# Kernel tuning notes

Measured on AMD Instinct MI355X. Metric: run time of the kernel, lower is better.

Reference implementation:

```python
import jax, jax.numpy as jnp
import numpy as np

N_NODES = 50000
N_EDGES = 1600000
D_FEAT = 128
EPS = 1e-12  # matches F.normalize clamp_min eps


def setup_inputs() -> dict:
    key = jax.random.key(0)
    k1, k2 = jax.random.split(key)
    x = jax.random.normal(k1, (N_NODES, D_FEAT), dtype=jnp.float32)
    beta = jnp.ones((1,), dtype=jnp.float32)  # AGNNConv learnable scalar, init 1.0
    edge_index = jax.random.randint(k2, (2, N_EDGES), 0, N_NODES, dtype=jnp.int64)
    return {"x": x, "beta": beta, "edge_index": edge_index}


def reference(x, beta, edge_index):
    N = x.shape[0]
    # AGNNConv default add_self_loops=True
    loop = jnp.arange(N, dtype=edge_index.dtype)
    src = jnp.concatenate([edge_index[0], loop])  # j (source / message sender)
    dst = jnp.concatenate([edge_index[1], loop])  # i (target / aggregator)

    # cosine-similarity attention logits per edge, scaled by beta
    xn = x * jax.lax.rsqrt(jnp.maximum(jnp.sum(x * x, axis=-1, keepdims=True), EPS * EPS))
    logits = beta[0] * jnp.sum(xn[src] * xn[dst], axis=-1)  # [E+N]

    # segment softmax over incoming edges of each target node
    m = jax.ops.segment_max(logits, dst, num_segments=N)
    m = jax.lax.stop_gradient(m)
    e = jnp.exp(logits - m[dst])
    s = jax.ops.segment_sum(e, dst, num_segments=N)
    alpha = e / s[dst]  # self-loops guarantee s > 0

    # scatter-aggregate messages alpha_e * x_src
    out = jax.ops.segment_sum(alpha[:, None] * x[src], dst, num_segments=N)

    # wrapper: activation (relu); normalization=False; dropout p=0 -> identity
    return jax.nn.relu(out)
```

## Files before the change

kernel.cpp:

```cpp
#include <hip/hip_runtime.h>

#define NN 50000
#define NE 1600000
#define DF 128
#define NB 1250
#define BSZ 40
#define CAP 1664
#define NWGP 512
#define CHKP 3125
#define NBF 3125

static __device__ __forceinline__ float bflo(unsigned int u) {
    unsigned int v = u << 16; float f; __builtin_memcpy(&f, &v, 4); return f;
}
static __device__ __forceinline__ float bfhi(unsigned int u) {
    unsigned int v = u & 0xFFFF0000u; float f; __builtin_memcpy(&f, &v, 4); return f;
}
static __device__ __forceinline__ unsigned int f2bf(float f) {
    unsigned int u; __builtin_memcpy(&u, &f, 4);
    u += 0x7FFFu + ((u >> 16) & 1u);
    return u >> 16;
}

static __device__ __forceinline__ int block_excl_scan512(int v, int t, int* wsum8) {
    int lane = t & 63, wv = t >> 6;
    int s = v;
    #pragma unroll
    for (int off = 1; off < 64; off <<= 1) {
        int u = __shfl_up(s, off);
        if (lane >= off) s += u;
    }
    if (lane == 63) wsum8[wv] = s;
    __syncthreads();
    int add = 0;
    #pragma unroll
    for (int w = 0; w < 8; ++w) add += (w < wv) ? wsum8[w] : 0;
    __syncthreads();
    return s + add - v;
}

static __device__ __forceinline__ int block_excl_scan256(int v, int t, int* wsum4) {
    int lane = t & 63, wv = t >> 6;
    int s = v;
    #pragma unroll
    for (int off = 1; off < 64; off <<= 1) {
        int u = __shfl_up(s, off);
        if (lane >= off) s += u;
    }
    if (lane == 63) wsum4[wv] = s;
    __syncthreads();
    int add = 0;
    #pragma unroll
    for (int w = 0; w < 4; ++w) add += (w < wv) ? wsum4[w] : 0;
    __syncthreads();
    return s + add - v;
}

__global__ __launch_bounds__(512)
void k_norm_part(const float* __restrict__ x,
                 const int* __restrict__ ei,
                 unsigned int* __restrict__ xn_bf,
                 float* __restrict__ norm,
                 unsigned int* __restrict__ descG,
                 unsigned int* __restrict__ pairs) {
    __shared__ int wsum8[8];
    __shared__ int cntL[NB];
    __shared__ int offL[NB];
    __shared__ unsigned int stg[CHKP];
    int t = threadIdx.x;
    if (blockIdx.x >= NWGP) {
        int nbid = blockIdx.x - NWGP;
        int l32 = t & 31;
        int node = nbid * 16 + ((t >> 6) << 1) + ((t & 63) >> 5);
        float4 v = ((const float4*)(x + (size_t)node * DF))[l32];
        float ss = v.x * v.x + v.y * v.y + v.z * v.z + v.w * v.w;
        #pragma unroll
        for (int m = 1; m < 32; m <<= 1) ss += __shfl_xor(ss, m);
        float rinv = rsqrtf(fmaxf(ss, 1e-24f));
        uint2 p;
        p.x = (f2bf(v.y * rinv) << 16) | f2bf(v.x * rinv);
        p.y = (f2bf(v.w * rinv) << 16) | f2bf(v.z * rinv);
        ((uint2*)(xn_bf + (size_t)node * 64))[l32] = p;
        if (l32 == 0) norm[node] = ss * rinv;
        return;
    }
    int wg = blockIdx.x;
    const int* srcp = ei + wg * CHKP;
    const int* dstp = ei + NE + wg * CHKP;
    for (int i = t; i < NB; i += 512) cntL[i] = 0;
    __syncthreads();
    #pragma unroll 4
    for (int i = t; i < CHKP; i += 512) atomicAdd(&cntL[dstp[i] / BSZ], 1);
    __syncthreads();
    {
        int base = t * 3;
        int loc[3];
        int s = 0;
        #pragma unroll
        for (int q = 0; q < 3; ++q) {
            int idx = base + q;
            int v = (idx < NB) ? cntL[idx] : 0;
            loc[q] = s;
            s += v;
        }
        int ex = block_excl_scan512(s, t, wsum8);
        #pragma unroll
        for (int q = 0; q < 3; ++q) {
            int idx = base + q;
            if (idx < NB) offL[idx] = ex + loc[q];
        }
    }
    __syncthreads();
    for (int i = t; i < NB; i += 512)
        descG[(size_t)wg * NB + i] = ((unsigned int)offL[i] << 16) | (unsigned int)cntL[i];
    __syncthreads();
    #pragma unroll 2
    for (int i = t; i < CHKP; i += 512) {
        int src = srcp[i];
        int dst = dstp[i];
        int b = dst / BSZ;
        int pos = atomicAdd(&offL[b], 1);
        stg[pos] = ((unsigned int)(dst - b * BSZ) << 16) | (unsigned int)src;
    }
    __syncthreads();
    unsigned int* chunk = pairs + (size_t)wg * CHKP;
    #pragma unroll 4
    for (int i = t; i < CHKP; i += 512) chunk[i] = stg[i];
}

__global__ __launch_bounds__(256)
void k_build_gather(const unsigned int* __restrict__ xn_bf,
                    const float* __restrict__ norm,
                    const unsigned int* __restrict__ descG,
                    const unsigned int* __restrict__ pairs,
                    const float* __restrict__ beta_p,
                    float* __restrict__ out) {
    __shared__ int wsum4[4];
    __shared__ int lenS[NWGP], offS[NWGP], rbase[NWGP];
    __shared__ unsigned int rawL[CAP];
    __shared__ unsigned int colL[CAP];
    __shared__ int hist[BSZ];
    __shared__ int rp[BSZ + 1];
    __shared__ int tot0, stotal;
    int b = blockIdx.x, t = threadIdx.x;

    unsigned int d0 = descG[(size_t)t * NB + b];
    unsigned int d1 = descG[(size_t)(t + 256) * NB + b];
    int len0 = (int)(d0 & 0xFFFFu), off0 = (int)(d0 >> 16);
    int len1 = (int)(d1 & 0xFFFFu), off1 = (int)(d1 >> 16);
    int rb0 = block_excl_scan256(len0, t, wsum4);
    if (t == 255) tot0 = rb0 + len0;
    int ex1 = block_excl_scan256(len1, t, wsum4);
    int rb1 = tot0 + ex1;
    if (t == 255) stotal = rb1 + len1;
    lenS[t] = len0;        offS[t] = off0;        rbase[t] = rb0;
    lenS[t + 256] = len1;  offS[t + 256] = off1;  rbase[t + 256] = rb1;
    if (t < BSZ) hist[t] = 0;
    __syncthreads();
    int cnt = stotal;
    if (cnt > CAP) cnt = CAP;

    int g16 = t >> 4, l16 = t & 15;
    for (int r = g16; r < NWGP; r += 16) {
        int len = lenS[r];
        int rb = rbase[r];
        const unsigned int* sp = pairs + (size_t)r * CHKP + offS[r];
        for (int q = l16; q < len; q += 16) {
            int pos = rb + q;
            if (pos < CAP) rawL[pos] = sp[q];
        }
    }
    __syncthreads();
    for (int i = t; i < cnt; i += 256) atomicAdd(&hist[rawL[i] >> 16], 1);
    __syncthreads();
    if (t < 64) {
        int v = (t < BSZ) ? hist[t] : 0;
        int s = v;
        #pragma unroll
        for (int off = 1; off < 64; off <<= 1) {
            int u = __shfl_up(s, off);
            if (t >= off) s += u;
        }
        if (t < BSZ) { rp[t + 1] = s; hist[t] = s - v; }
        if (t == 0) rp[0] = 0;
    }
    __syncthreads();
    for (int i = t; i < cnt; i += 256) {
        unsigned int p = rawL[i];
        unsigned int src = p & 0xFFFFu;
        int pos = atomicAdd(&hist[p >> 16], 1);
        colL[pos] = (f2bf(norm[src]) << 16) | src;
    }
    __syncthreads();

    int lane = t & 63;
    int w = t >> 6;
    int j = lane & 15;
    int g = lane >> 4;
    float beta = beta_p[0];
    float c = -fabsf(beta);
    for (int ln = w; ln < BSZ; ln += 4) {
        int node = b * BSZ + ln;
        uint4 du = ((const uint4*)(xn_bf + (size_t)node * 64))[j];
        float xd[8];
        #pragma unroll
        for (int q = 0; q < 4; ++q) {
            unsigned int u = (&du.x)[q];
            xd[2 * q]     = bflo(u);
            xd[2 * q + 1] = bfhi(u);
        }
        float acc[8] = {0.f, 0.f, 0.f, 0.f, 0.f, 0.f, 0.f, 0.f};
        float ssum = 0.f;
        int b0 = rp[ln], b1 = rp[ln + 1];

        int k = b0 + g;
        int kA = (k     < b1) ? k     : 0;
        int kB = (k + 4 < b1) ? k + 4 : 0;
        unsigned int pA = colL[kA];
        unsigned int pB = colL[kB];
        uint4 rA = ((const uint4*)(xn_bf + (size_t)(pA & 0xFFFFu) * 64))[j];
        uint4 rB = ((const uint4*)(xn_bf + (size_t)(pB & 0xFFFFu) * 64))[j];

        for (; k < b1; k += 8) {
            int kC = (k +  8 < b1) ? k +  8 : 0;
            int kD = (k + 12 < b1) ? k + 12 : 0;
            unsigned int pC = colL[kC];
            unsigned int pD = colL[kD];
            uint4 rC = ((const uint4*)(xn_bf + (size_t)(pC & 0xFFFFu) * 64))[j];
            uint4 rD = ((const uint4*)(xn_bf + (size_t)(pD & 0xFFFFu) * 64))[j];
            {
                float xs[8];
                #pragma unroll
                for (int q = 0; q < 4; ++q) {
                    unsigned int u = (&rA.x)[q];
                    xs[2 * q]     = bflo(u);
                    xs[2 * q + 1] = bfhi(u);
                }
                float dot = 0.f;
                #pragma unroll
                for (int q = 0; q < 8; ++q) dot = fmaf(xd[q], xs[q], dot);
                dot += __shfl_xor(dot, 1);
                dot += __shfl_xor(dot, 2);
                dot += __shfl_xor(dot, 4);
                dot += __shfl_xor(dot, 8);
                float e = __expf(fmaf(beta, dot, c));
                ssum += e;
                float wgt = e * bfhi(pA);
                #pragma unroll
                for (int q = 0; q < 8; ++q) acc[q] = fmaf(wgt, xs[q], acc[q]);
            }
            {
                float xs[8];
                #pragma unroll
                for (int q = 0; q < 4; ++q) {
                    unsigned int u = (&rB.x)[q];
                    xs[2 * q]     = bflo(u);
                    xs[2 * q + 1] = bfhi(u);
                }
                float dot = 0.f;
                #pragma unroll
                for (int q = 0; q < 8; ++q) dot = fmaf(xd[q], xs[q], dot);
                dot += __shfl_xor(dot, 1);
                dot += __shfl_xor(dot, 2);
                dot += __shfl_xor(dot, 4);
                dot += __shfl_xor(dot, 8);
                float e = __expf(fmaf(beta, dot, c));
                e = (k + 4 < b1) ? e : 0.f;
                ssum += e;
                float wgt = e * bfhi(pB);
                #pragma unroll
                for (int q = 0; q < 8; ++q) acc[q] = fmaf(wgt, xs[q], acc[q]);
            }
            pA = pC; pB = pD; rA = rC; rB = rD;
        }

        ssum += __shfl_xor(ssum, 16);
        ssum += __shfl_xor(ssum, 32);
        #pragma unroll
        for (int q = 0; q < 8; ++q) {
            acc[q] += __shfl_xor(acc[q], 16);
            acc[q] += __shfl_xor(acc[q], 32);
        }
        float e_self = __expf(beta + c);
        ssum += e_self;
        float wsl = e_self * norm[node];
        #pragma unroll
        for (int q = 0; q < 8; ++q) acc[q] = fmaf(wsl, xd[q], acc[q]);

        if (g == 0) {
            float inv = 1.0f / ssum;
            float4 o0, o1;
            o0.x = fmaxf(0.f, acc[0] * inv); o0.y = fmaxf(0.f, acc[1] * inv);
            o0.z = fmaxf(0.f, acc[2] * inv); o0.w = fmaxf(0.f, acc[3] * inv);
            o1.x = fmaxf(0.f, acc[4] * inv); o1.y = fmaxf(0.f, acc[5] * inv);
            o1.z = fmaxf(0.f, acc[6] * inv); o1.w = fmaxf(0.f, acc[7] * inv);
            float4* op = (float4*)(out + (size_t)node * DF + 8 * j);
            op[0] = o0;
            op[1] = o1;
        }
    }
}

extern "C" void kernel_launch(void* const* d_in, const int* in_sizes, int n_in,
                              void* d_out, int out_size, void* d_ws, size_t ws_size,
                              hipStream_t stream) {
    const float* x    = (const float*)d_in[0];
    const float* beta = (const float*)d_in[1];
    const int*   ei   = (const int*)d_in[2];
    float*       out  = (float*)d_out;

    char* ws = (char*)d_ws;
    unsigned int* xn_bf = (unsigned int*)ws;
    float* norm = (float*)(ws + 12800000);
    unsigned int* descG = (unsigned int*)(ws + 13000000);
    unsigned int* pairs = (unsigned int*)(ws + 15560000);

    k_norm_part  <<<NWGP + NBF, 512, 0, stream>>>(x, ei, xn_bf, norm, descG, pairs);
    k_build_gather<<<NB,        256, 0, stream>>>(xn_bf, norm, descG, pairs, beta, out);
}
```

Measured before the change: 162.1 us.

## Coarsen edge partition to 64 chunks and split normalization into own kernel

```diff
diff --git a/kernel.cpp b/kernel.cpp
--- a/kernel.cpp
+++ b/kernel.cpp
@@ -6,8 +6,8 @@
 #define NB 1250
 #define BSZ 40
 #define CAP 1664
-#define NWGP 512
-#define CHKP 3125
+#define NWGP 64
+#define CHKP 25000
 #define NBF 3125
 
 static __device__ __forceinline__ float bflo(unsigned int u) {
@@ -39,52 +39,15 @@
     return s + add - v;
 }
 
-static __device__ __forceinline__ int block_excl_scan256(int v, int t, int* wsum4) {
-    int lane = t & 63, wv = t >> 6;
-    int s = v;
-    #pragma unroll
-    for (int off = 1; off < 64; off <<= 1) {
-        int u = __shfl_up(s, off);
-        if (lane >= off) s += u;
-    }
-    if (lane == 63) wsum4[wv] = s;
-    __syncthreads();
-    int add = 0;
-    #pragma unroll
-    for (int w = 0; w < 4; ++w) add += (w < wv) ? wsum4[w] : 0;
-    __syncthreads();
-    return s + add - v;
-}
-
 __global__ __launch_bounds__(512)
-void k_norm_part(const float* __restrict__ x,
-                 const int* __restrict__ ei,
-                 unsigned int* __restrict__ xn_bf,
-                 float* __restrict__ norm,
-                 unsigned int* __restrict__ descG,
-                 unsigned int* __restrict__ pairs) {
+void k_part(const int* __restrict__ ei,
+            unsigned int* __restrict__ descG,
+            unsigned int* __restrict__ pairs) {
     __shared__ int wsum8[8];
     __shared__ int cntL[NB];
     __shared__ int offL[NB];
     __shared__ unsigned int stg[CHKP];
-    int t = threadIdx.x;
-    if (blockIdx.x >= NWGP) {
-        int nbid = blockIdx.x - NWGP;
-        int l32 = t & 31;
-        int node = nbid * 16 + ((t >> 6) << 1) + ((t & 63) >> 5);
-        float4 v = ((const float4*)(x + (size_t)node * DF))[l32];
-        float ss = v.x * v.x + v.y * v.y + v.z * v.z + v.w * v.w;
-        #pragma unroll
-        for (int m = 1; m < 32; m <<= 1) ss += __shfl_xor(ss, m);
-        float rinv = rsqrtf(fmaxf(ss, 1e-24f));
-        uint2 p;
-        p.x = (f2bf(v.y * rinv) << 16) | f2bf(v.x * rinv);
-        p.y = (f2bf(v.w * rinv) << 16) | f2bf(v.z * rinv);
-        ((uint2*)(xn_bf + (size_t)node * 64))[l32] = p;
-        if (l32 == 0) norm[node] = ss * rinv;
-        return;
-    }
-    int wg = blockIdx.x;
+    int wg = blockIdx.x, t = threadIdx.x;
     const int* srcp = ei + wg * CHKP;
     const int* dstp = ei + NE + wg * CHKP;
     for (int i = t; i < NB; i += 512) cntL[i] = 0;
@@ -128,6 +91,25 @@
     for (int i = t; i < CHKP; i += 512) chunk[i] = stg[i];
 }
 
+__global__ __launch_bounds__(512)
+void k_norm(const float* __restrict__ x,
+            unsigned int* __restrict__ xn_bf,
+            float* __restrict__ norm) {
+    int t = threadIdx.x;
+    int l32 = t & 31;
+    int node = blockIdx.x * 16 + (t >> 5);
+    float4 v = ((const float4*)(x + (size_t)node * DF))[l32];
+    float ss = v.x * v.x + v.y * v.y + v.z * v.z + v.w * v.w;
+    #pragma unroll
+    for (int m = 1; m < 32; m <<= 1) ss += __shfl_xor(ss, m);
+    float rinv = rsqrtf(fmaxf(ss, 1e-24f));
+    uint2 p;
+    p.x = (f2bf(v.y * rinv) << 16) | f2bf(v.x * rinv);
+    p.y = (f2bf(v.w * rinv) << 16) | f2bf(v.z * rinv);
+    ((uint2*)(xn_bf + (size_t)node * 64))[l32] = p;
+    if (l32 == 0) norm[node] = ss * rinv;
+}
+
 __global__ __launch_bounds__(256)
 void k_build_gather(const unsigned int* __restrict__ xn_bf,
                     const float* __restrict__ norm,
@@ -135,29 +117,31 @@
                     const unsigned int* __restrict__ pairs,
                     const float* __restrict__ beta_p,
                     float* __restrict__ out) {
-    __shared__ int wsum4[4];
     __shared__ int lenS[NWGP], offS[NWGP], rbase[NWGP];
     __shared__ unsigned int rawL[CAP];
     __shared__ unsigned int colL[CAP];
     __shared__ int hist[BSZ];
     __shared__ int rp[BSZ + 1];
-    __shared__ int tot0, stotal;
+    __shared__ int stot;
     int b = blockIdx.x, t = threadIdx.x;
 
-    unsigned int d0 = descG[(size_t)t * NB + b];
-    unsigned int d1 = descG[(size_t)(t + 256) * NB + b];
-    int len0 = (int)(d0 & 0xFFFFu), off0 = (int)(d0 >> 16);
-    int len1 = (int)(d1 & 0xFFFFu), off1 = (int)(d1 >> 16);
-    int rb0 = block_excl_scan256(len0, t, wsum4);
-    if (t == 255) tot0 = rb0 + len0;
-    int ex1 = block_excl_scan256(len1, t, wsum4);
-    int rb1 = tot0 + ex1;
-    if (t == 255) stotal = rb1 + len1;
-    lenS[t] = len0;        offS[t] = off0;        rbase[t] = rb0;
-    lenS[t + 256] = len1;  offS[t + 256] = off1;  rbase[t + 256] = rb1;
-    if (t < BSZ) hist[t] = 0;
-    __syncthreads();
-    int cnt = stotal;
+    if (t < NWGP) {
+        unsigned int d = descG[(size_t)t * NB + b];
+        int len = (int)(d & 0xFFFFu);
+        int s = len;
+        #pragma unroll
+        for (int off = 1; off < 64; off <<= 1) {
+            int u = __shfl_up(s, off);
+            if (t >= off) s += u;
+        }
+        lenS[t] = len;
+        offS[t] = (int)(d >> 16);
+        rbase[t] = s - len;
+        if (t == NWGP - 1) stot = s;
+    }
+    if (t >= 64 && t < 64 + BSZ) hist[t - 64] = 0;
+    __syncthreads();
+    int cnt = stot;
     if (cnt > CAP) cnt = CAP;
 
     int g16 = t >> 4, l16 = t & 15;
@@ -313,8 +297,9 @@
     unsigned int* xn_bf = (unsigned int*)ws;
     float* norm = (float*)(ws + 12800000);
     unsigned int* descG = (unsigned int*)(ws + 13000000);
-    unsigned int* pairs = (unsigned int*)(ws + 15560000);
-
-    k_norm_part  <<<NWGP + NBF, 512, 0, stream>>>(x, ei, xn_bf, norm, descG, pairs);
-    k_build_gather<<<NB,        256, 0, stream>>>(xn_bf, norm, descG, pairs, beta, out);
-}
+    unsigned int* pairs = (unsigned int*)(ws + 13320000);
+
+    k_part        <<<NWGP, 512, 0, stream>>>(ei, descG, pairs);
+    k_norm        <<<NBF,  512, 0, stream>>>(x, xn_bf, norm);
+    k_build_gather<<<NB,   256, 0, stream>>>(xn_bf, norm, descG, pairs, beta, out);
+}
```

After: 177.6 us. 9.5% more time.
